# Optimization experiments

Hardware: AMD Instinct MI355X
Metric: run time of the kernel (lower is better)

## Reference

```python
import jax, jax.numpy as jnp
import numpy as np

EMB = 1024

def setup_inputs() -> dict:
    key = jax.random.key(0)
    ks = jax.random.split(key, 7)
    s = 1.0 / np.sqrt(EMB)
    x = jax.random.normal(ks[0], (4, 2048, EMB), dtype=jnp.float32)
    Wk = jax.random.normal(ks[1], (EMB, EMB), dtype=jnp.float32) * s
    bk = jnp.zeros((EMB,), dtype=jnp.float32)
    Wq = jax.random.normal(ks[2], (EMB, EMB), dtype=jnp.float32) * s
    bq = jnp.zeros((EMB,), dtype=jnp.float32)
    Wv = jax.random.normal(ks[3], (EMB, EMB), dtype=jnp.float32) * s
    bv = jnp.zeros((EMB,), dtype=jnp.float32)
    return {"x": x, "Wk": Wk, "bk": bk, "Wq": Wq, "bq": bq, "Wv": Wv, "bv": bv}

def reference(x, Wk, bk, Wq, bq, Wv, bv):
    # Linear layers: x @ W.T + b (torch nn.Linear convention)
    k = jnp.einsum('bse,fe->bsf', x, Wk) + bk
    q = jnp.einsum('bse,fe->bsf', x, Wq) + bq
    v = jnp.einsum('bse,fe->bsf', x, Wv) + bv
    E = x.shape[-1]
    # NOTE: original computes k @ q^T (not q @ k^T) — reproduce faithfully.
    sim = jnp.einsum('bsd,btd->bst', k, q) / jnp.sqrt(jnp.float32(E))
    S = x.shape[1]
    causal = jnp.tril(jnp.ones((S, S), dtype=bool))  # [S,S]
    sim = jnp.where(causal, sim, -jnp.inf)
    attn = jax.nn.softmax(sim, axis=-1)
    return jnp.einsum('bst,btd->bsd', attn, v)
```

## Files before the change

### kernel.cpp

```cpp
#include <hip/hip_runtime.h>
#include <cstdint>


typedef __attribute__((ext_vector_type(8))) _Float16 f16x8;
typedef __attribute__((ext_vector_type(4))) float f32x4;

__device__ __forceinline__ unsigned short f2h(float x) {
  return __builtin_bit_cast(unsigned short, (_Float16)x);
}

__device__ __forceinline__ void lds_dma16(const void* g, void* l) {
  auto gp = reinterpret_cast<const __attribute__((address_space(1))) void*>(
      reinterpret_cast<uintptr_t>(g));
  auto lp = reinterpret_cast<__attribute__((address_space(3))) void*>(
      reinterpret_cast<uintptr_t>(l));
  __builtin_amdgcn_global_load_lds(gp, lp, 16, 0, 0);
}

__device__ __forceinline__ void gemm128(const unsigned short* __restrict__ Ag,
                                        const unsigned short* __restrict__ Bg,
                                        int lda, int ldb, int nk,
                                        unsigned short* As, unsigned short* Bs,
                                        f32x4 acc[4][4]) {
  const int tid = threadIdx.x;
  const int lane = tid & 63, wave = tid >> 6;
  const int wm = wave >> 1, wn = wave & 1;
  const int sr = lane >> 3;
  const int scb = ((lane & 7) ^ sr) * 8;
  const int rr = lane & 15, qq = lane >> 4;
  const int slot0 = ((qq) ^ (rr & 7)) * 8;
  const int slot1 = ((4 + qq) ^ (rr & 7)) * 8;

#pragma unroll
  for (int i = 0; i < 4; ++i)
#pragma unroll
    for (int j = 0; j < 4; ++j) {
      f32x4 z = {0.f, 0.f, 0.f, 0.f};
      acc[i][j] = z;
    }

  for (int k0 = 0; k0 < nk; k0 += 64) {
#pragma unroll
    for (int c = 0; c < 4; ++c) {
      int chunk = wave * 4 + c;
      int row = chunk * 8 + sr;
      lds_dma16(Ag + (size_t)row * lda + k0 + scb, As + chunk * 512);
      lds_dma16(Bg + (size_t)row * ldb + k0 + scb, Bs + chunk * 512);
    }
    __syncthreads();

    const unsigned short* Ar = As + (wm * 64 + rr) * 64;
    const unsigned short* Br = Bs + (wn * 64 + rr) * 64;
    {
      f16x8 af[4], bf[4];
#pragma unroll
      for (int i = 0; i < 4; ++i) af[i] = *(const f16x8*)(Ar + i * 1024 + slot0);
#pragma unroll
      for (int j = 0; j < 4; ++j) bf[j] = *(const f16x8*)(Br + j * 1024 + slot0);
#pragma unroll
      for (int i = 0; i < 4; ++i)
#pragma unroll
        for (int j = 0; j < 4; ++j)
          acc[i][j] = __builtin_amdgcn_mfma_f32_16x16x32_f16(af[i], bf[j],
                                                             acc[i][j], 0, 0, 0);
    }
    {
      f16x8 af[4], bf[4];
#pragma unroll
      for (int i = 0; i < 4; ++i) af[i] = *(const f16x8*)(Ar + i * 1024 + slot1);
#pragma unroll
      for (int j = 0; j < 4; ++j) bf[j] = *(const f16x8*)(Br + j * 1024 + slot1);
#pragma unroll
      for (int i = 0; i < 4; ++i)
#pragma unroll
        for (int j = 0; j < 4; ++j)
          acc[i][j] = __builtin_amdgcn_mfma_f32_16x16x32_f16(af[i], bf[j],
                                                             acc[i][j], 0, 0, 0);
    }
    __syncthreads();
  }
}

__global__ void cvt_kernel(const float* __restrict__ x,
                           const float* __restrict__ w0,
                           const float* __restrict__ w1,
                           const float* __restrict__ w2,
                           unsigned short* __restrict__ dst,
                           float* __restrict__ rsum) {
  int i = blockIdx.x * 256 + threadIdx.x;
  if (i >= 2883584) {
    int z2 = i - 2883584;
    float4 z = {0.f, 0.f, 0.f, 0.f};
    ((float4*)rsum)[z2] = z;
    return;
  }
  const float* s;
  size_t si;
  if (i < 2097152) {
    s = x; si = i;
  } else {
    int j = i - 2097152;
    int z = j >> 18;
    s = (z == 0) ? w0 : ((z == 1) ? w1 : w2);
    si = j & 262143;
  }
  float4 f = ((const float4*)s)[si];
  ushort4 u;
  u.x = f2h(f.x); u.y = f2h(f.y); u.z = f2h(f.z); u.w = f2h(f.w);
  ((ushort4*)dst)[i] = u;
}

__global__ __launch_bounds__(256) void qkv_gemm_kernel(
    const unsigned short* __restrict__ xh, const unsigned short* __restrict__ wh,
    const float* __restrict__ bk, const float* __restrict__ bq,
    const float* __restrict__ bv, unsigned short* __restrict__ kh,
    unsigned short* __restrict__ qh, unsigned short* __restrict__ vh) {
  __shared__ unsigned short As[128 * 64], Bs[128 * 64];
  const int tn = blockIdx.x & 7, z = blockIdx.x >> 3;
  const unsigned short* W = wh + (size_t)z * 1048576;
  const float* bias = (z == 0) ? bk : ((z == 1) ? bq : bv);
  unsigned short* dst = (z == 0) ? kh : ((z == 1) ? qh : vh);
  const int tm = blockIdx.y;

  f32x4 acc[4][4];
  gemm128(xh + (size_t)tm * 128 * 1024, W + (size_t)tn * 128 * 1024,
          1024, 1024, 1024, As, Bs, acc);

  const int lane = threadIdx.x & 63, wave = threadIdx.x >> 6;
  const int wm = wave >> 1, wn = wave & 1, rr = lane & 15, qq = lane >> 4;
  float bj[4];
#pragma unroll
  for (int j = 0; j < 4; ++j)
    bj[j] = bias[tn * 128 + wn * 64 + j * 16 + rr];
#pragma unroll
  for (int i = 0; i < 4; ++i)
#pragma unroll
    for (int reg = 0; reg < 4; ++reg) {
      int gm = tm * 128 + wm * 64 + i * 16 + qq * 4 + reg;
#pragma unroll
      for (int j = 0; j < 4; ++j) {
        int gc = tn * 128 + wn * 64 + j * 16 + rr;
        dst[(size_t)gm * 1024 + gc] = f2h(acc[i][j][reg] + bj[j]);
      }
    }
}

__global__ __launch_bounds__(256) void transpose_v_kernel(
    const unsigned short* __restrict__ v, unsigned short* __restrict__ vT) {
  __shared__ unsigned short tile[64][65];
  const int b = blockIdx.z;
  const unsigned short* vp = v + (size_t)b * 2048 * 1024;
  unsigned short* vtp = vT + (size_t)b * 1024 * 2048;
  const int t0 = blockIdx.x * 64, d0 = blockIdx.y * 64;
  const int lr = threadIdx.x >> 4, lc = (threadIdx.x & 15) * 4;
#pragma unroll
  for (int p = 0; p < 4; ++p) {
    int tr = p * 16 + lr;
    ushort4 u = *(const ushort4*)(vp + (size_t)(t0 + tr) * 1024 + d0 + lc);
    tile[tr][lc] = u.x; tile[tr][lc + 1] = u.y;
    tile[tr][lc + 2] = u.z; tile[tr][lc + 3] = u.w;
  }
  __syncthreads();
#pragma unroll
  for (int p = 0; p < 4; ++p) {
    int dr = p * 16 + lr;
    ushort4 u;
    u.x = tile[lc][dr]; u.y = tile[lc + 1][dr];
    u.z = tile[lc + 2][dr]; u.w = tile[lc + 3][dr];
    *(ushort4*)(vtp + (size_t)(d0 + dr) * 2048 + t0 + lc) = u;
  }
}

__global__ __launch_bounds__(256) void scores_kernel(
    const unsigned short* __restrict__ kh, const unsigned short* __restrict__ qh,
    unsigned short* __restrict__ P, float* __restrict__ rsum) {
  const int b = blockIdx.y;
  int idx = blockIdx.x;
  int ts = (int)((sqrtf(8.0f * idx + 1.0f) - 1.0f) * 0.5f);
  while ((ts + 1) * (ts + 2) / 2 <= idx) ++ts;
  while (ts * (ts + 1) / 2 > idx) --ts;
  const int tt = idx - ts * (ts + 1) / 2;
  __shared__ unsigned short As[128 * 64], Bs[128 * 64];

  f32x4 acc[4][4];
  gemm128(kh + ((size_t)(b * 2048 + ts * 128)) * 1024,
          qh + ((size_t)(b * 2048 + tt * 128)) * 1024,
          1024, 1024, 1024, As, Bs, acc);

  const int lane = threadIdx.x & 63, wave = threadIdx.x >> 6;
  const int wm = wave >> 1, wn = wave & 1, rr = lane & 15, qq = lane >> 4;
  unsigned short* Pb = P + (size_t)b * 2048 * 2048;
  float* rs = rsum + b * 2048;
#pragma unroll
  for (int i = 0; i < 4; ++i)
#pragma unroll
    for (int reg = 0; reg < 4; ++reg) {
      int srow = ts * 128 + wm * 64 + i * 16 + qq * 4 + reg;
      float p = 0.f;
#pragma unroll
      for (int j = 0; j < 4; ++j) {
        int tcol = tt * 128 + wn * 64 + j * 16 + rr;
        float e = (tcol <= srow) ? __expf(acc[i][j][reg] * 0.03125f - 4.0f)
                                 : 0.0f;
        Pb[(size_t)srow * 2048 + tcol] = f2h(e);
        p += e;
      }
#pragma unroll
      for (int off = 1; off < 16; off <<= 1) p += __shfl_xor(p, off);
      if (rr == 0) atomicAdd(rs + srow, p);
    }
}

__global__ __launch_bounds__(256) void pv_gemm_kernel(
    const unsigned short* __restrict__ P, const unsigned short* __restrict__ vT,
    const float* __restrict__ rsum, float* __restrict__ out) {
  const int td = blockIdx.x, ts = 15 - blockIdx.y, b = blockIdx.z;
  __shared__ unsigned short As[128 * 64], Bs[128 * 64];

  f32x4 acc[4][4];
  gemm128(P + ((size_t)(b * 2048 + ts * 128)) * 2048,
          vT + ((size_t)(b * 1024 + td * 128)) * 2048,
          2048, 2048, (ts + 1) * 128, As, Bs, acc);

  const int lane = threadIdx.x & 63, wave = threadIdx.x >> 6;
  const int wm = wave >> 1, wn = wave & 1, rr = lane & 15, qq = lane >> 4;
#pragma unroll
  for (int i = 0; i < 4; ++i)
#pragma unroll
    for (int reg = 0; reg < 4; ++reg) {
      int srow = ts * 128 + wm * 64 + i * 16 + qq * 4 + reg;
      float rv = __builtin_amdgcn_rcpf(rsum[b * 2048 + srow]);
#pragma unroll
      for (int j = 0; j < 4; ++j) {
        int dcol = td * 128 + wn * 64 + j * 16 + rr;
        out[((size_t)(b * 2048 + srow)) * 1024 + dcol] = acc[i][j][reg] * rv;
      }
    }
}

extern "C" void kernel_launch(void* const* d_in, const int* in_sizes, int n_in,
                              void* d_out, int out_size, void* d_ws,
                              size_t ws_size, hipStream_t stream) {
  const float* x  = (const float*)d_in[0];
  const float* Wk = (const float*)d_in[1];
  const float* bk = (const float*)d_in[2];
  const float* Wq = (const float*)d_in[3];
  const float* bq = (const float*)d_in[4];
  const float* Wv = (const float*)d_in[5];
  const float* bv = (const float*)d_in[6];
  float* out = (float*)d_out;

  char* ws = (char*)d_ws;
  const size_t MB = 1ull << 20;
  unsigned short* xh = (unsigned short*)(ws + 0);
  unsigned short* wh = (unsigned short*)(ws + 16 * MB);
  unsigned short* vh = (unsigned short*)(ws + 22 * MB);
  unsigned short* P  = (unsigned short*)(ws + 0);
  unsigned short* kh = (unsigned short*)(ws + 38 * MB);
  unsigned short* qh = (unsigned short*)(ws + 54 * MB);
  unsigned short* vT = (unsigned short*)(ws + 70 * MB);
  float* rsum = (float*)(ws + 86 * MB);

  cvt_kernel<<<11272, 256, 0, stream>>>(x, Wk, Wq, Wv, xh, rsum);
  qkv_gemm_kernel<<<dim3(24, 64), 256, 0, stream>>>(xh, wh, bk, bq, bv,
                                                    kh, qh, vh);
  transpose_v_kernel<<<dim3(32, 16, 4), 256, 0, stream>>>(vh, vT);
  scores_kernel<<<dim3(136, 4), 256, 0, stream>>>(kh, qh, P, rsum);
  pv_gemm_kernel<<<dim3(8, 16, 4), 256, 0, stream>>>(P, vT, rsum, out);
}
```

Before: 266.9 us.

## Double-buffer LDS tiles in shared GEMM with K-step of 32

Restructures the shared 128x128 GEMM mainloop to use two LDS buffers with a K-step of 32 instead of a single 64-wide buffer. The DMA for the next K slice is issued before computing on the current one, so global-to-LDS loads overlap with MFMA work, and one of the two barriers per iteration is removed. The swizzle pattern is redone for the 32-wide rows. In exchange, each iteration does half as much MFMA work per barrier, so barrier and loop overhead per FLOP doubles, and the global_load_lds latency may not be fully hidden at this depth.

```diff
diff --git a/kernel.cpp b/kernel.cpp
--- a/kernel.cpp
+++ b/kernel.cpp
@@ -25,11 +25,10 @@
   const int tid = threadIdx.x;
   const int lane = tid & 63, wave = tid >> 6;
   const int wm = wave >> 1, wn = wave & 1;
-  const int sr = lane >> 3;
-  const int scb = ((lane & 7) ^ sr) * 8;
+  const int sr = lane >> 2;
+  const int scb = (((lane & 3) ^ ((lane >> 3) & 3)) * 8);
   const int rr = lane & 15, qq = lane >> 4;
-  const int slot0 = ((qq) ^ (rr & 7)) * 8;
-  const int slot1 = ((4 + qq) ^ (rr & 7)) * 8;
+  const int slot = ((qq ^ ((rr >> 1) & 3)) * 8);
 
 #pragma unroll
   for (int i = 0; i < 4; ++i)
@@ -39,45 +38,46 @@
       acc[i][j] = z;
     }
 
-  for (int k0 = 0; k0 < nk; k0 += 64) {
-#pragma unroll
-    for (int c = 0; c < 4; ++c) {
-      int chunk = wave * 4 + c;
-      int row = chunk * 8 + sr;
-      lds_dma16(Ag + (size_t)row * lda + k0 + scb, As + chunk * 512);
-      lds_dma16(Bg + (size_t)row * ldb + k0 + scb, Bs + chunk * 512);
-    }
+  const int srow_a = (wave * 2) * 16 + sr;
+#pragma unroll
+  for (int c = 0; c < 2; ++c) {
+    int chunk = wave * 2 + c;
+    int row = chunk * 16 + sr;
+    lds_dma16(Ag + (size_t)row * lda + scb, As + chunk * 512);
+    lds_dma16(Bg + (size_t)row * ldb + scb, Bs + chunk * 512);
+  }
+  (void)srow_a;
+
+  int buf = 0;
+  for (int k0 = 0; k0 < nk; k0 += 32) {
     __syncthreads();
-
-    const unsigned short* Ar = As + (wm * 64 + rr) * 64;
-    const unsigned short* Br = Bs + (wn * 64 + rr) * 64;
-    {
-      f16x8 af[4], bf[4];
-#pragma unroll
-      for (int i = 0; i < 4; ++i) af[i] = *(const f16x8*)(Ar + i * 1024 + slot0);
-#pragma unroll
-      for (int j = 0; j < 4; ++j) bf[j] = *(const f16x8*)(Br + j * 1024 + slot0);
-#pragma unroll
-      for (int i = 0; i < 4; ++i)
-#pragma unroll
-        for (int j = 0; j < 4; ++j)
-          acc[i][j] = __builtin_amdgcn_mfma_f32_16x16x32_f16(af[i], bf[j],
-                                                             acc[i][j], 0, 0, 0);
-    }
-    {
-      f16x8 af[4], bf[4];
-#pragma unroll
-      for (int i = 0; i < 4; ++i) af[i] = *(const f16x8*)(Ar + i * 1024 + slot1);
-#pragma unroll
-      for (int j = 0; j < 4; ++j) bf[j] = *(const f16x8*)(Br + j * 1024 + slot1);
-#pragma unroll
-      for (int i = 0; i < 4; ++i)
-#pragma unroll
-        for (int j = 0; j < 4; ++j)
-          acc[i][j] = __builtin_amdgcn_mfma_f32_16x16x32_f16(af[i], bf[j],
-                                                             acc[i][j], 0, 0, 0);
-    }
-    __syncthreads();
+    const int kn = k0 + 32;
+    if (kn < nk) {
+      unsigned short* An = As + (buf ^ 1) * 4096;
+      unsigned short* Bn = Bs + (buf ^ 1) * 4096;
+#pragma unroll
+      for (int c = 0; c < 2; ++c) {
+        int chunk = wave * 2 + c;
+        int row = chunk * 16 + sr;
+        lds_dma16(Ag + (size_t)row * lda + kn + scb, An + chunk * 512);
+        lds_dma16(Bg + (size_t)row * ldb + kn + scb, Bn + chunk * 512);
+      }
+    }
+
+    f16x8 af[4], bf[4];
+    const unsigned short* Ar = As + buf * 4096 + (wm * 64 + rr) * 32 + slot;
+    const unsigned short* Br = Bs + buf * 4096 + (wn * 64 + rr) * 32 + slot;
+#pragma unroll
+    for (int i = 0; i < 4; ++i) af[i] = *(const f16x8*)(Ar + i * 512);
+#pragma unroll
+    for (int j = 0; j < 4; ++j) bf[j] = *(const f16x8*)(Br + j * 512);
+#pragma unroll
+    for (int i = 0; i < 4; ++i)
+#pragma unroll
+      for (int j = 0; j < 4; ++j)
+        acc[i][j] = __builtin_amdgcn_mfma_f32_16x16x32_f16(af[i], bf[j],
+                                                           acc[i][j], 0, 0, 0);
+    buf ^= 1;
   }
 }
 
@@ -115,7 +115,7 @@
     const float* __restrict__ bk, const float* __restrict__ bq,
     const float* __restrict__ bv, unsigned short* __restrict__ kh,
     unsigned short* __restrict__ qh, unsigned short* __restrict__ vh) {
-  __shared__ unsigned short As[128 * 64], Bs[128 * 64];
+  __shared__ unsigned short As[2 * 128 * 32], Bs[2 * 128 * 32];
   const int tn = blockIdx.x & 7, z = blockIdx.x >> 3;
   const unsigned short* W = wh + (size_t)z * 1048576;
   const float* bias = (z == 0) ? bk : ((z == 1) ? bq : bv);
@@ -180,7 +180,7 @@
   while ((ts + 1) * (ts + 2) / 2 <= idx) ++ts;
   while (ts * (ts + 1) / 2 > idx) --ts;
   const int tt = idx - ts * (ts + 1) / 2;
-  __shared__ unsigned short As[128 * 64], Bs[128 * 64];
+  __shared__ unsigned short As[2 * 128 * 32], Bs[2 * 128 * 32];
 
   f32x4 acc[4][4];
   gemm128(kh + ((size_t)(b * 2048 + ts * 128)) * 1024,
@@ -215,7 +215,7 @@
     const unsigned short* __restrict__ P, const unsigned short* __restrict__ vT,
     const float* __restrict__ rsum, float* __restrict__ out) {
   const int td = blockIdx.x, ts = 15 - blockIdx.y, b = blockIdx.z;
-  __shared__ unsigned short As[128 * 64], Bs[128 * 64];
+  __shared__ unsigned short As[2 * 128 * 32], Bs[2 * 128 * 32];
 
   f32x4 acc[4][4];
   gemm128(P + ((size_t)(b * 2048 + ts * 128)) * 2048,
```

Result: faster. 250.6 us (-6.1%).
